# Kernel optimization log

Measured on AMD Instinct MI355X. Metric: run time of the kernel, lower is better.

The kernel has to match this reference:

```python
import jax, jax.numpy as jnp
import numpy as np
import math

B, S, H = 2, 2048, 4096
NH, HD = 32, 128            # num_heads, head_dim
Q_RANK, KV_RANK = 1536, 512 # low-rank dims
VD = 128                    # v_head_dim


def setup_inputs() -> dict:
    key = jax.random.key(0)
    ks = jax.random.split(key, 7)
    s = 0.02
    return {
        "hidden_states": jax.random.normal(ks[0], (B, S, H), dtype=jnp.float32),
        "w_qa":  jax.random.normal(ks[1], (H, Q_RANK), dtype=jnp.float32) * s,
        "w_qb":  jax.random.normal(ks[2], (Q_RANK, NH * HD), dtype=jnp.float32) * s,
        "w_kva": jax.random.normal(ks[3], (H, KV_RANK), dtype=jnp.float32) * s,
        "w_kb":  jax.random.normal(ks[4], (KV_RANK, NH * HD), dtype=jnp.float32) * s,
        "w_vb":  jax.random.normal(ks[5], (KV_RANK, NH * VD), dtype=jnp.float32) * s,
        "w_o":   jax.random.normal(ks[6], (NH * VD, H), dtype=jnp.float32) * s,
    }


def reference(hidden_states, w_qa, w_qb, w_kva, w_kb, w_vb, w_o):
    b, s, _ = hidden_states.shape
    # low-rank Q path
    q_c = hidden_states @ w_qa                       # [B,S,q_rank]
    q = (q_c @ w_qb).reshape(b, s, NH, HD)           # [B,S,NH,HD]
    # low-rank compressed KV (this is the cache tensor)
    compressed_kv = hidden_states @ w_kva            # [B,S,kv_rank]
    k = (compressed_kv @ w_kb).reshape(b, s, NH, HD)
    v = (compressed_kv @ w_vb).reshape(b, s, NH, VD)
    # causal SDPA, scale 1/sqrt(head_dim) (position_ids=None -> RoPE no-op)
    scale = 1.0 / math.sqrt(HD)
    scores = jnp.einsum('bqhd,bkhd->bhqk', q, k) * scale
    causal = jnp.tril(jnp.ones((s, s), dtype=bool))
    scores = jnp.where(causal, scores, jnp.finfo(scores.dtype).min)
    attn = jax.nn.softmax(scores, axis=-1)
    out = jnp.einsum('bhqk,bkhd->bqhd', attn, v).reshape(b, s, NH * VD)
    attn_output = out @ w_o                          # [B,S,H]
    return (attn_output, compressed_kv)
```

## Files before the change

### kernel.cpp

```cpp
#include <hip/hip_runtime.h>
#include <hip/hip_bf16.h>
#include <math.h>

#define BB 2
#define SS 2048
#define HH 4096
#define NHEADS 32
#define HDIM 128
#define VDIM 128
#define QRANK 1536
#define KVRANK 512
#define MROWS (BB * SS)

typedef unsigned short u16;
typedef unsigned int u32;
typedef short short8 __attribute__((ext_vector_type(8)));
typedef float floatx4 __attribute__((ext_vector_type(4)));

#if __has_builtin(__builtin_amdgcn_exp2f)
__device__ __forceinline__ float fast_exp2(float x) { return __builtin_amdgcn_exp2f(x); }
#else
__device__ __forceinline__ float fast_exp2(float x) { return exp2f(x); }
#endif

__device__ __forceinline__ u16 f2bf(float f) {
    u32 u = __float_as_uint(f);
    u += 0x7fffu + ((u >> 16) & 1u);
    return (u16)(u >> 16);
}

#define GLD16(gp, lp)                                                        \
    __builtin_amdgcn_global_load_lds(                                        \
        (const __attribute__((address_space(1))) void*)(gp),                 \
        (__attribute__((address_space(3))) void*)(lp), 16, 0, 0)

__global__ __launch_bounds__(256) void cvt_bf16(const float* __restrict__ in,
                                                u16* __restrict__ out, int n4) {
    int idx = blockIdx.x * 256 + threadIdx.x;
    int stride = gridDim.x * 256;
    for (int i = idx; i < n4; i += stride) {
        float4 f = ((const float4*)in)[i];
        u32 lo = (u32)f2bf(f.x) | ((u32)f2bf(f.y) << 16);
        u32 hi = (u32)f2bf(f.z) | ((u32)f2bf(f.w) << 16);
        ((uint2*)out)[i] = make_uint2(lo, hi);
    }
}

__global__ __launch_bounds__(256) void transpose_cvt(const float* __restrict__ in,
                                                     u16* __restrict__ out,
                                                     int R, int C) {
    __shared__ u16 T[64][65];
    const int c0 = blockIdx.x * 64, r0 = blockIdx.y * 64;
    const int tx = threadIdx.x & 63, ty = threadIdx.x >> 6;
#pragma unroll
    for (int p = 0; p < 16; ++p) {
        int rr = p * 4 + ty;
        T[rr][tx] = f2bf(in[(size_t)(r0 + rr) * C + c0 + tx]);
    }
    __syncthreads();
#pragma unroll
    for (int p = 0; p < 16; ++p) {
        int cc = p * 4 + ty;
        out[(size_t)(c0 + cc) * R + r0 + tx] = T[tx][cc];
    }
}

__global__ __launch_bounds__(256) void transpose_v(const u16* __restrict__ in, int ldin,
                                                   u16* __restrict__ out) {
    __shared__ u16 T[64][65];
    const int s0 = blockIdx.x * 64, d0 = blockIdx.y * 64;
    const int bh = blockIdx.z, b = bh >> 5, h = bh & 31;
    const int tx = threadIdx.x & 63, ty = threadIdx.x >> 6;
#pragma unroll
    for (int p = 0; p < 16; ++p) {
        int ss = p * 4 + ty;
        T[ss][tx] = in[(size_t)(b * SS + s0 + ss) * ldin + h * 128 + d0 + tx];
    }
    __syncthreads();
#pragma unroll
    for (int p = 0; p < 16; ++p) {
        int dd = p * 4 + ty;
        out[((size_t)bh * 128 + d0 + dd) * SS + s0 + tx] = T[tx][dd];
    }
}

template <int MODE>
__global__ __launch_bounds__(512) void gemm_bt(const u16* __restrict__ A, int lda,
                                               const u16* __restrict__ Bt, int ldb,
                                               float* __restrict__ Cf, int ldf,
                                               u16* __restrict__ Cb, int ldc,
                                               int M, int N, int K, int nsplit) {
    __shared__ __align__(16) u16 As[4][256 * 32];
    __shared__ __align__(16) u16 Bs[4][256 * 32];

    const int tid = threadIdx.x;
    const int bm0 = blockIdx.y * 256, bn0 = blockIdx.x * 256;
    const int w = tid >> 6, lane = tid & 63;
    const int lo = lane & 15, quad = lane >> 4;
    const int wm = (w >> 2) * 128, wn = (w & 3) * 64;

    floatx4 acc[8][4];
#pragma unroll
    for (int m = 0; m < 8; ++m)
#pragma unroll
        for (int n = 0; n < 4; ++n) acc[m][n] = (floatx4){0.f, 0.f, 0.f, 0.f};

    int row_[2], gco[2], ldso[2];
#pragma unroll
    for (int p = 0; p < 2; ++p) {
        int o = tid * 16 + p * 8192;
        row_[p] = o >> 6;
        int c = (o & 63) >> 4;
        gco[p] = ((c ^ ((row_[p] >> 1) & 3)) << 3);
        ldso[p] = o >> 1;
    }

    const u16* Ab = A + (size_t)bm0 * lda;
    const u16* Bb = Bt + (size_t)bn0 * ldb;
    const int NT = K >> 5;

    auto STAGE = [&](int t) {
        const int s = t & 3;
        const int k0 = t << 5;
#pragma unroll
        for (int p = 0; p < 2; ++p)
            GLD16(Ab + (size_t)row_[p] * lda + k0 + gco[p], &As[s][ldso[p]]);
#pragma unroll
        for (int p = 0; p < 2; ++p)
            GLD16(Bb + (size_t)row_[p] * ldb + k0 + gco[p], &Bs[s][ldso[p]]);
    };

    STAGE(0);
    if (NT > 1) STAGE(1);
    if (NT > 2) STAGE(2);

    for (int kt = 0; kt < NT; ++kt) {
        __builtin_amdgcn_s_barrier();
        if (kt + 3 < NT) STAGE(kt + 3);
        __builtin_amdgcn_sched_barrier(0);
        if (kt < NT - 3)       asm volatile("s_waitcnt vmcnt(12)" ::: "memory");
        else if (kt == NT - 3) asm volatile("s_waitcnt vmcnt(8)" ::: "memory");
        else if (kt == NT - 2) asm volatile("s_waitcnt vmcnt(4)" ::: "memory");
        else                   asm volatile("s_waitcnt vmcnt(0)" ::: "memory");
        __builtin_amdgcn_sched_barrier(0);
        __builtin_amdgcn_s_barrier();
        __builtin_amdgcn_sched_barrier(0);

        const int s = kt & 3;
        short8 af[8], bfr[4];
#pragma unroll
        for (int m = 0; m < 8; ++m) {
            const int r = wm + m * 16 + lo;
            af[m] = *(const short8*)&As[s][r * 32 + ((quad ^ ((r >> 1) & 3)) << 3)];
        }
#pragma unroll
        for (int n = 0; n < 4; ++n) {
            const int r = wn + n * 16 + lo;
            bfr[n] = *(const short8*)&Bs[s][r * 32 + ((quad ^ ((r >> 1) & 3)) << 3)];
        }
        __builtin_amdgcn_s_setprio(1);
#pragma unroll
        for (int m = 0; m < 8; ++m)
#pragma unroll
            for (int n = 0; n < 4; ++n)
                acc[m][n] = __builtin_amdgcn_mfma_f32_16x16x32_bf16(af[m], bfr[n], acc[m][n], 0, 0, 0);
        __builtin_amdgcn_s_setprio(0);
    }

#pragma unroll
    for (int m = 0; m < 8; ++m) {
#pragma unroll
        for (int n = 0; n < 4; ++n) {
            const int row = bm0 + wm + m * 16 + quad * 4;
            const int col = bn0 + wn + n * 16 + lo;
#pragma unroll
            for (int r = 0; r < 4; ++r) {
                float v = acc[m][n][r];
                if (MODE == 0) Cf[(size_t)(row + r) * ldf + col] = v;
                if (MODE == 1) Cb[(size_t)(row + r) * ldc + col] = f2bf(v);
                if (MODE == 3) {
                    Cb[(size_t)(row + r) * ldc + col] = f2bf(v);
                    if (col >= nsplit) Cf[(size_t)(row + r) * ldf + (col - nsplit)] = v;
                }
            }
        }
    }
}

__global__ __launch_bounds__(256) void mla_attn_mfma(const u16* __restrict__ qm,
                                                     const u16* __restrict__ km, int ldk,
                                                     const u16* __restrict__ vt,
                                                     u16* __restrict__ ao) {
    __shared__ __align__(16) u16 Ks[64 * 128];
    __shared__ __align__(16) u16 Vt[(128 + 16) * 64];
    __shared__ __align__(16) u16 Ps[128 * 68];

    const int qt = 15 - blockIdx.y;
    const int bh = blockIdx.x;
    const int b = bh >> 5, h = bh & 31;
    const int tid = threadIdx.x;
    const int w = tid >> 6, lane = tid & 63;
    const int lo = lane & 15, quad = lane >> 4;
    const int q0 = qt * 128;

    const float SCALE_L2E = 0.08838834764831845f * 1.4426950408889634f;

    {
        u32* p = (u32*)&Vt[128 * 64];
        for (int i = tid; i < 512; i += 256) p[i] = 0x3F803F80u;
    }

    const u16* kbase = km + (size_t)(b * SS) * ldk + h * 128;
    const u16* vtbase = vt + (size_t)bh * 128 * SS;
    const int nkt = 2 * qt + 2;

    int ol_[4], kgo[4], vgo[4];
#pragma unroll
    for (int p = 0; p < 4; ++p) {
        int o = tid * 16 + p * 4096;
        int key = o >> 8, ch = (o & 255) >> 4;
        kgo[p] = key * ldk + ((ch ^ (key & 15)) << 3);
        int d = o >> 7, ch2 = (o & 127) >> 4;
        vgo[p] = d * SS + ((ch2 ^ (d & 7)) << 3);
        ol_[p] = o >> 1;
    }

#pragma unroll
    for (int p = 0; p < 4; ++p) GLD16(kbase + kgo[p], &Ks[ol_[p]]);
#pragma unroll
    for (int p = 0; p < 4; ++p) GLD16(vtbase + vgo[p], &Vt[ol_[p]]);

    short8 qf[2][4];
#pragma unroll
    for (int mf = 0; mf < 2; ++mf) {
        const u16* qrow = qm + (size_t)(b * SS + q0 + w * 32 + mf * 16 + lo) * HH + h * 128;
#pragma unroll
        for (int ks = 0; ks < 4; ++ks) qf[mf][ks] = *(const short8*)(qrow + ks * 32 + quad * 8);
    }

    floatx4 oacc[2][8], olv[2];
#pragma unroll
    for (int mf = 0; mf < 2; ++mf) {
        olv[mf] = (floatx4){0.f, 0.f, 0.f, 0.f};
#pragma unroll
        for (int n = 0; n < 8; ++n) oacc[mf][n] = (floatx4){0.f, 0.f, 0.f, 0.f};
    }

    __syncthreads();

    for (int kt = 0; kt < nkt; ++kt) {
        const bool need_mask = (kt >= nkt - 2);
        const bool notlast = (kt + 1 < nkt);

#pragma unroll
        for (int mf = 0; mf < 2; ++mf) {
            floatx4 s[4];
#pragma unroll
            for (int nf = 0; nf < 4; ++nf) s[nf] = (floatx4){0.f, 0.f, 0.f, 0.f};
            __builtin_amdgcn_s_setprio(1);
#pragma unroll
            for (int nf = 0; nf < 4; ++nf)
#pragma unroll
                for (int ks = 0; ks < 4; ++ks) {
                    short8 kf = *(const short8*)&Ks[(nf * 16 + lo) * 128 + (((ks * 4 + quad) ^ lo) << 3)];
                    s[nf] = __builtin_amdgcn_mfma_f32_16x16x32_bf16(qf[mf][ks], kf, s[nf], 0, 0, 0);
                }
            __builtin_amdgcn_s_setprio(0);
#pragma unroll
            for (int nf = 0; nf < 4; ++nf)
#pragma unroll
                for (int r = 0; r < 4; ++r) {
                    float p = fast_exp2(s[nf][r] * SCALE_L2E);
                    if (need_mask) {
                        int kgi = kt * 64 + nf * 16 + lo;
                        int qg = q0 + w * 32 + mf * 16 + quad * 4 + r;
                        p = (kgi <= qg) ? p : 0.f;
                    }
                    Ps[(w * 32 + mf * 16 + quad * 4 + r) * 68 + nf * 16 + lo] = f2bf(p);
                }
        }

        __syncthreads();

        if (notlast) {
            const u16* kn = kbase + (size_t)(kt + 1) * 64 * ldk;
#pragma unroll
            for (int p = 0; p < 4; ++p) GLD16(kn + kgo[p], &Ks[ol_[p]]);
        }

#pragma unroll
        for (int mf = 0; mf < 2; ++mf) {
            short8 pa[2];
#pragma unroll
            for (int ks2 = 0; ks2 < 2; ++ks2)
                pa[ks2] = *(const short8*)&Ps[(w * 32 + mf * 16 + lo) * 68 + ks2 * 32 + quad * 8];
            __builtin_amdgcn_s_setprio(1);
#pragma unroll
            for (int n = 0; n < 8; ++n)
#pragma unroll
                for (int ks2 = 0; ks2 < 2; ++ks2) {
                    short8 vf = *(const short8*)&Vt[(n * 16 + lo) * 64 + (((ks2 * 4 + quad) ^ (lo & 7)) << 3)];
                    oacc[mf][n] = __builtin_amdgcn_mfma_f32_16x16x32_bf16(pa[ks2], vf, oacc[mf][n], 0, 0, 0);
                }
#pragma unroll
            for (int ks2 = 0; ks2 < 2; ++ks2) {
                short8 vf = *(const short8*)&Vt[(128 + lo) * 64 + (((ks2 * 4 + quad) ^ (lo & 7)) << 3)];
                olv[mf] = __builtin_amdgcn_mfma_f32_16x16x32_bf16(pa[ks2], vf, olv[mf], 0, 0, 0);
            }
            __builtin_amdgcn_s_setprio(0);
        }

        __syncthreads();

        if (notlast) {
            const u16* vn = vtbase + (size_t)(kt + 1) * 64;
#pragma unroll
            for (int p = 0; p < 4; ++p) GLD16(vn + vgo[p], &Vt[ol_[p]]);
        }
    }

#pragma unroll
    for (int mf = 0; mf < 2; ++mf) {
        u16* obase = ao + (size_t)(b * SS + q0 + w * 32 + mf * 16 + quad * 4) * HH + h * 128;
#pragma unroll
        for (int r = 0; r < 4; ++r) {
            float inv = 1.f / olv[mf][r];
#pragma unroll
            for (int n = 0; n < 8; ++n)
                obase[(size_t)r * HH + n * 16 + lo] = f2bf(oacc[mf][n][r] * inv);
        }
    }
}

extern "C" void kernel_launch(void* const* d_in, const int* in_sizes, int n_in,
                              void* d_out, int out_size, void* d_ws, size_t ws_size,
                              hipStream_t stream) {
    const float* hs    = (const float*)d_in[0];
    const float* w_qa  = (const float*)d_in[1];
    const float* w_qb  = (const float*)d_in[2];
    const float* w_kva = (const float*)d_in[3];
    const float* w_kb  = (const float*)d_in[4];
    const float* w_vb  = (const float*)d_in[5];
    const float* w_o   = (const float*)d_in[6];

    float* out   = (float*)d_out;
    float* ckv_f = out + (size_t)MROWS * HH;

    u16* ws = (u16*)d_ws;
    u16* hs_bf    = ws;
    u16* vt       = ws;
    u16* q_bf     = ws + 16777216ull;
    u16* kv_bf    = ws + 33554432ull;
    u16* ao_bf    = ws + 67108864ull;
    u16* wqa_kvaT = ws + 83886080ull;
    u16* w_qbT    = ws + 92274688ull;
    u16* wkv_bT   = ws + 98566144ull;
    u16* w_oT     = ws + 102760448ull;
    u16* qc_ckv   = ws + 119537664ull;

    dim3 blk(256);
    dim3 blkg(512);

    cvt_bf16<<<2048, blk, 0, stream>>>(hs, hs_bf, (MROWS * HH) / 4);
    transpose_cvt<<<dim3(QRANK / 64, HH / 64), blk, 0, stream>>>(w_qa, wqa_kvaT, HH, QRANK);
    transpose_cvt<<<dim3(KVRANK / 64, HH / 64), blk, 0, stream>>>(w_kva, wqa_kvaT + 1536ull * 4096, HH, KVRANK);
    transpose_cvt<<<dim3(HH / 64, QRANK / 64), blk, 0, stream>>>(w_qb, w_qbT, QRANK, HH);
    transpose_cvt<<<dim3(HH / 64, KVRANK / 64), blk, 0, stream>>>(w_kb, wkv_bT, KVRANK, HH);
    transpose_cvt<<<dim3(HH / 64, KVRANK / 64), blk, 0, stream>>>(w_vb, wkv_bT + 4096ull * 512, KVRANK, HH);
    transpose_cvt<<<dim3(HH / 64, HH / 64), blk, 0, stream>>>(w_o, w_oT, HH, HH);

    gemm_bt<3><<<dim3(2048 / 256, MROWS / 256), blkg, 0, stream>>>(
        hs_bf, HH, wqa_kvaT, HH, ckv_f, KVRANK, qc_ckv, 2048, MROWS, 2048, HH, QRANK);
    gemm_bt<1><<<dim3(HH / 256, MROWS / 256), blkg, 0, stream>>>(
        qc_ckv, 2048, w_qbT, QRANK, nullptr, 0, q_bf, HH, MROWS, HH, QRANK, 0);
    gemm_bt<1><<<dim3(8192 / 256, MROWS / 256), blkg, 0, stream>>>(
        qc_ckv + 1536, 2048, wkv_bT, KVRANK, nullptr, 0, kv_bf, 8192, MROWS, 8192, KVRANK, 0);
    transpose_v<<<dim3(SS / 64, VDIM / 64, BB * NHEADS), blk, 0, stream>>>(kv_bf + 4096, 8192, vt);
    mla_attn_mfma<<<dim3(BB * NHEADS, 16), blk, 0, stream>>>(q_bf, kv_bf, 8192, vt, ao_bf);
    gemm_bt<0><<<dim3(HH / 256, MROWS / 256), blkg, 0, stream>>>(
        ao_bf, HH, w_oT, HH, out, HH, nullptr, 0, MROWS, HH, HH, 0);
}
```

Measured before the change: 799.2 us.

## Restructure bf16 GEMM mainloop into 4-phase ping-pong with 64-wide K tiles

Measured after the change: 788.1 us. Within noise of the previous version (-1.4%).

```diff
diff --git a/kernel.cpp b/kernel.cpp
--- a/kernel.cpp
+++ b/kernel.cpp
@@ -84,19 +84,75 @@
     }
 }
 
+#define PHASE_BAR(NLIT)                                                          \
+    __builtin_amdgcn_sched_barrier(0);                                           \
+    asm volatile("s_waitcnt vmcnt(" NLIT ")\n\ts_barrier" ::: "memory");         \
+    __builtin_amdgcn_sched_barrier(0)
+
+#define MFMA_Q(AH, BH, AFR, BFR)                                                 \
+    __builtin_amdgcn_s_setprio(1);                                               \
+    _Pragma("unroll") for (int m_ = 0; m_ < 4; ++m_)                             \
+    _Pragma("unroll") for (int n_ = 0; n_ < 2; ++n_)                             \
+    _Pragma("unroll") for (int ks_ = 0; ks_ < 2; ++ks_)                          \
+        acc[m_ + (AH)*4][n_ + (BH)*2] = __builtin_amdgcn_mfma_f32_16x16x32_bf16( \
+            AFR[m_][ks_], BFR[n_][ks_], acc[m_ + (AH)*4][n_ + (BH)*2], 0, 0, 0); \
+    __builtin_amdgcn_s_setprio(0);                                               \
+    __builtin_amdgcn_sched_barrier(0)
+
+#define GTILE(T, WL)                                                              \
+    {                                                                             \
+        const int slot = (T) & 1;                                                 \
+        short8 a0[4][2], a1[4][2], b0[2][2], b1[2][2];                            \
+               \
+        _Pragma("unroll") for (int m_ = 0; m_ < 4; ++m_)                          \
+        _Pragma("unroll") for (int ks_ = 0; ks_ < 2; ++ks_)                       \
+            a0[m_][ks_] = *(const short8*)&As[slot][(wm + m_ * 16 + lo) * 64 +    \
+                                                    (((ks_ * 4 + quad) ^ lo7) << 3)]; \
+        _Pragma("unroll") for (int n_ = 0; n_ < 2; ++n_)                          \
+        _Pragma("unroll") for (int ks_ = 0; ks_ < 2; ++ks_)                       \
+            b0[n_][ks_] = *(const short8*)&Bs[slot][(wn + n_ * 16 + lo) * 64 +    \
+                                                    (((ks_ * 4 + quad) ^ lo7) << 3)]; \
+        if ((T) > 0 && (T) + 1 < NT) STAGE_A((T) + 1, 1);                         \
+        PHASE_BAR(WL);                                                            \
+        MFMA_Q(0, 0, a0, b0);                                                     \
+        asm volatile("s_waitcnt lgkmcnt(0)\n\ts_barrier" ::: "memory");           \
+        __builtin_amdgcn_sched_barrier(0);                                        \
+                       \
+        _Pragma("unroll") for (int n_ = 0; n_ < 2; ++n_)                          \
+        _Pragma("unroll") for (int ks_ = 0; ks_ < 2; ++ks_)                       \
+            b1[n_][ks_] = *(const short8*)&Bs[slot][(wn + 32 + n_ * 16 + lo) * 64 + \
+                                                    (((ks_ * 4 + quad) ^ lo7) << 3)]; \
+        if ((T) + 2 < NT) STAGE_A((T) + 2, 0);                                    \
+        PHASE_BAR(WL);                                                            \
+        MFMA_Q(0, 1, a0, b1);                                                     \
+                       \
+        _Pragma("unroll") for (int m_ = 0; m_ < 4; ++m_)                          \
+        _Pragma("unroll") for (int ks_ = 0; ks_ < 2; ++ks_)                       \
+            a1[m_][ks_] = *(const short8*)&As[slot][(wm + 64 + m_ * 16 + lo) * 64 + \
+                                                    (((ks_ * 4 + quad) ^ lo7) << 3)]; \
+        if ((T) + 2 < NT) STAGE_B((T) + 2, 0);                                    \
+        PHASE_BAR(WL);                                                            \
+        MFMA_Q(1, 0, a1, b0);                                                     \
+                                   \
+        if ((T) + 2 < NT) STAGE_B((T) + 2, 1);                                    \
+        PHASE_BAR(WL);                                                            \
+        MFMA_Q(1, 1, a1, b1);                                                     \
+    }
+
 template <int MODE>
 __global__ __launch_bounds__(512) void gemm_bt(const u16* __restrict__ A, int lda,
                                                const u16* __restrict__ Bt, int ldb,
                                                float* __restrict__ Cf, int ldf,
                                                u16* __restrict__ Cb, int ldc,
                                                int M, int N, int K, int nsplit) {
-    __shared__ __align__(16) u16 As[4][256 * 32];
-    __shared__ __align__(16) u16 Bs[4][256 * 32];
+    __shared__ __align__(16) u16 As[2][256 * 64];
+    __shared__ __align__(16) u16 Bs[2][256 * 64];
 
     const int tid = threadIdx.x;
     const int bm0 = blockIdx.y * 256, bn0 = blockIdx.x * 256;
     const int w = tid >> 6, lane = tid & 63;
     const int lo = lane & 15, quad = lane >> 4;
+    const int lo7 = lane & 7, l8 = lane >> 3;
     const int wm = (w >> 2) * 128, wn = (w & 3) * 64;
 
     floatx4 acc[8][4];
@@ -104,68 +160,50 @@
     for (int m = 0; m < 8; ++m)
 #pragma unroll
         for (int n = 0; n < 4; ++n) acc[m][n] = (floatx4){0.f, 0.f, 0.f, 0.f};
-
-    int row_[2], gco[2], ldso[2];
-#pragma unroll
-    for (int p = 0; p < 2; ++p) {
-        int o = tid * 16 + p * 8192;
-        row_[p] = o >> 6;
-        int c = (o & 63) >> 4;
-        gco[p] = ((c ^ ((row_[p] >> 1) & 3)) << 3);
-        ldso[p] = o >> 1;
-    }
 
     const u16* Ab = A + (size_t)bm0 * lda;
     const u16* Bb = Bt + (size_t)bn0 * ldb;
-    const int NT = K >> 5;
-
-    auto STAGE = [&](int t) {
-        const int s = t & 3;
-        const int k0 = t << 5;
+    const int NT = K >> 6;
+
+    const u16* aSrc[2][2]; const u16* bSrc[2][2];
+    int aDst[2][2], bDst[2][2];
+    const int csw = (lo7 ^ l8) << 3;
+#pragma unroll
+    for (int p = 0; p < 2; ++p) {
+        const int idx = w * 2 + p;
+#pragma unroll
+        for (int P = 0; P < 2; ++P) {
+            const int ra = (idx >> 3) * 128 + (idx & 7) * 8 + P * 64;
+            aSrc[P][p] = Ab + (size_t)(ra + l8) * lda + csw;
+            aDst[P][p] = ra * 64 + lane * 8;
+            const int rb = (idx >> 2) * 64 + (idx & 3) * 8 + P * 32;
+            bSrc[P][p] = Bb + (size_t)(rb + l8) * ldb + csw;
+            bDst[P][p] = rb * 64 + lane * 8;
+        }
+    }
+
+    auto STAGE_A = [&](int t, int P) {
+        const int s = t & 1;
 #pragma unroll
         for (int p = 0; p < 2; ++p)
-            GLD16(Ab + (size_t)row_[p] * lda + k0 + gco[p], &As[s][ldso[p]]);
+            GLD16(aSrc[P][p] + t * 64, &As[s][aDst[P][p]]);
+    };
+    auto STAGE_B = [&](int t, int P) {
+        const int s = t & 1;
 #pragma unroll
         for (int p = 0; p < 2; ++p)
-            GLD16(Bb + (size_t)row_[p] * ldb + k0 + gco[p], &Bs[s][ldso[p]]);
+            GLD16(bSrc[P][p] + t * 64, &Bs[s][bDst[P][p]]);
     };
 
-    STAGE(0);
-    if (NT > 1) STAGE(1);
-    if (NT > 2) STAGE(2);
-
-    for (int kt = 0; kt < NT; ++kt) {
-        __builtin_amdgcn_s_barrier();
-        if (kt + 3 < NT) STAGE(kt + 3);
-        __builtin_amdgcn_sched_barrier(0);
-        if (kt < NT - 3)       asm volatile("s_waitcnt vmcnt(12)" ::: "memory");
-        else if (kt == NT - 3) asm volatile("s_waitcnt vmcnt(8)" ::: "memory");
-        else if (kt == NT - 2) asm volatile("s_waitcnt vmcnt(4)" ::: "memory");
-        else                   asm volatile("s_waitcnt vmcnt(0)" ::: "memory");
-        __builtin_amdgcn_sched_barrier(0);
-        __builtin_amdgcn_s_barrier();
-        __builtin_amdgcn_sched_barrier(0);
-
-        const int s = kt & 3;
-        short8 af[8], bfr[4];
-#pragma unroll
-        for (int m = 0; m < 8; ++m) {
-            const int r = wm + m * 16 + lo;
-            af[m] = *(const short8*)&As[s][r * 32 + ((quad ^ ((r >> 1) & 3)) << 3)];
-        }
-#pragma unroll
-        for (int n = 0; n < 4; ++n) {
-            const int r = wn + n * 16 + lo;
-            bfr[n] = *(const short8*)&Bs[s][r * 32 + ((quad ^ ((r >> 1) & 3)) << 3)];
-        }
-        __builtin_amdgcn_s_setprio(1);
-#pragma unroll
-        for (int m = 0; m < 8; ++m)
-#pragma unroll
-            for (int n = 0; n < 4; ++n)
-                acc[m][n] = __builtin_amdgcn_mfma_f32_16x16x32_bf16(af[m], bfr[n], acc[m][n], 0, 0, 0);
-        __builtin_amdgcn_s_setprio(0);
-    }
+    STAGE_A(0, 0); STAGE_A(0, 1); STAGE_B(0, 0); STAGE_B(0, 1);
+    if (NT > 1) { STAGE_A(1, 0); STAGE_A(1, 1); STAGE_B(1, 0); STAGE_B(1, 1); }
+    asm volatile("s_waitcnt vmcnt(0)" ::: "memory");
+    __builtin_amdgcn_s_barrier();
+    __builtin_amdgcn_sched_barrier(0);
+
+    int t = 0;
+    for (; t + 2 < NT; ++t) GTILE(t, "10");
+    for (; t < NT; ++t) GTILE(t, "0");
 
 #pragma unroll
     for (int m = 0; m < 8; ++m) {
```

## Restructure GEMM mainloop into 8-phase ping-pong schedule with BK=64 tiles

Applied to the files above, without the earlier changes.

Result: faster. 693.4 us (-13.2%).

```diff
diff --git a/kernel.cpp b/kernel.cpp
--- a/kernel.cpp
+++ b/kernel.cpp
@@ -84,19 +84,33 @@
     }
 }
 
+#define BARRIER() asm volatile("s_barrier" ::: "memory")
+#define LGKM0()                                              \
+    asm volatile("s_waitcnt lgkmcnt(0)" ::: "memory");       \
+    __builtin_amdgcn_sched_barrier(0)
+#define MF16(MO, NO, AA, BB2)                                                     \
+    __builtin_amdgcn_s_setprio(1);                                                \
+    _Pragma("unroll") for (int m_ = 0; m_ < 4; ++m_)                              \
+    _Pragma("unroll") for (int n_ = 0; n_ < 2; ++n_)                              \
+    _Pragma("unroll") for (int k_ = 0; k_ < 2; ++k_)                              \
+        acc[m_ + (MO)][n_ + (NO)] = __builtin_amdgcn_mfma_f32_16x16x32_bf16(      \
+            AA[m_][k_], BB2[n_][k_], acc[m_ + (MO)][n_ + (NO)], 0, 0, 0);         \
+    __builtin_amdgcn_s_setprio(0)
+
 template <int MODE>
 __global__ __launch_bounds__(512) void gemm_bt(const u16* __restrict__ A, int lda,
                                                const u16* __restrict__ Bt, int ldb,
                                                float* __restrict__ Cf, int ldf,
                                                u16* __restrict__ Cb, int ldc,
                                                int M, int N, int K, int nsplit) {
-    __shared__ __align__(16) u16 As[4][256 * 32];
-    __shared__ __align__(16) u16 Bs[4][256 * 32];
+    __shared__ __align__(16) u16 As[2][256 * 64];
+    __shared__ __align__(16) u16 Bs[2][256 * 64];
 
     const int tid = threadIdx.x;
     const int bm0 = blockIdx.y * 256, bn0 = blockIdx.x * 256;
     const int w = tid >> 6, lane = tid & 63;
     const int lo = lane & 15, quad = lane >> 4;
+    const int lo7 = lane & 7, l8 = lane >> 3;
     const int wm = (w >> 2) * 128, wn = (w & 3) * 64;
 
     floatx4 acc[8][4];
@@ -104,67 +118,102 @@
     for (int m = 0; m < 8; ++m)
 #pragma unroll
         for (int n = 0; n < 4; ++n) acc[m][n] = (floatx4){0.f, 0.f, 0.f, 0.f};
-
-    int row_[2], gco[2], ldso[2];
-#pragma unroll
-    for (int p = 0; p < 2; ++p) {
-        int o = tid * 16 + p * 8192;
-        row_[p] = o >> 6;
-        int c = (o & 63) >> 4;
-        gco[p] = ((c ^ ((row_[p] >> 1) & 3)) << 3);
-        ldso[p] = o >> 1;
-    }
 
     const u16* Ab = A + (size_t)bm0 * lda;
     const u16* Bb = Bt + (size_t)bn0 * ldb;
-    const int NT = K >> 5;
-
-    auto STAGE = [&](int t) {
-        const int s = t & 3;
-        const int k0 = t << 5;
-#pragma unroll
-        for (int p = 0; p < 2; ++p)
-            GLD16(Ab + (size_t)row_[p] * lda + k0 + gco[p], &As[s][ldso[p]]);
-#pragma unroll
-        for (int p = 0; p < 2; ++p)
-            GLD16(Bb + (size_t)row_[p] * ldb + k0 + gco[p], &Bs[s][ldso[p]]);
+    const int NT = K >> 6;
+    const int csw = (lo7 ^ l8) << 3;
+
+    auto STAGE_A = [&](int s, int P, int tau) {
+#pragma unroll
+        for (int j = 0; j < 2; ++j) {
+            const int rb = P * 64 + j * 128 + w * 8;
+            GLD16(Ab + (size_t)(rb + l8) * lda + tau * 64 + csw, &As[s][rb * 64 + lane * 8]);
+        }
     };
-
-    STAGE(0);
-    if (NT > 1) STAGE(1);
-    if (NT > 2) STAGE(2);
-
-    for (int kt = 0; kt < NT; ++kt) {
-        __builtin_amdgcn_s_barrier();
-        if (kt + 3 < NT) STAGE(kt + 3);
-        __builtin_amdgcn_sched_barrier(0);
-        if (kt < NT - 3)       asm volatile("s_waitcnt vmcnt(12)" ::: "memory");
-        else if (kt == NT - 3) asm volatile("s_waitcnt vmcnt(8)" ::: "memory");
-        else if (kt == NT - 2) asm volatile("s_waitcnt vmcnt(4)" ::: "memory");
-        else                   asm volatile("s_waitcnt vmcnt(0)" ::: "memory");
-        __builtin_amdgcn_sched_barrier(0);
-        __builtin_amdgcn_s_barrier();
-        __builtin_amdgcn_sched_barrier(0);
-
-        const int s = kt & 3;
-        short8 af[8], bfr[4];
-#pragma unroll
-        for (int m = 0; m < 8; ++m) {
-            const int r = wm + m * 16 + lo;
-            af[m] = *(const short8*)&As[s][r * 32 + ((quad ^ ((r >> 1) & 3)) << 3)];
-        }
-#pragma unroll
-        for (int n = 0; n < 4; ++n) {
-            const int r = wn + n * 16 + lo;
-            bfr[n] = *(const short8*)&Bs[s][r * 32 + ((quad ^ ((r >> 1) & 3)) << 3)];
-        }
-        __builtin_amdgcn_s_setprio(1);
-#pragma unroll
-        for (int m = 0; m < 8; ++m)
-#pragma unroll
-            for (int n = 0; n < 4; ++n)
-                acc[m][n] = __builtin_amdgcn_mfma_f32_16x16x32_bf16(af[m], bfr[n], acc[m][n], 0, 0, 0);
-        __builtin_amdgcn_s_setprio(0);
+    auto STAGE_B = [&](int s, int P, int tau) {
+#pragma unroll
+        for (int j = 0; j < 2; ++j) {
+            const int rb = (w >> 2) * 64 + (w & 3) * 8 + P * 32 + j * 128;
+            GLD16(Bb + (size_t)(rb + l8) * ldb + tau * 64 + csw, &Bs[s][rb * 64 + lane * 8]);
+        }
+    };
+    auto RD_A = [&](short8 (&dst)[4][2], int s, int half) {
+#pragma unroll
+        for (int m = 0; m < 4; ++m)
+#pragma unroll
+            for (int ks = 0; ks < 2; ++ks) {
+                const int r = wm + half * 64 + m * 16 + lo;
+                dst[m][ks] = *(const short8*)&As[s][r * 64 + (((ks * 4 + quad) ^ lo7) << 3)];
+            }
+    };
+    auto RD_B = [&](short8 (&dst)[2][2], int s, int half) {
+#pragma unroll
+        for (int n = 0; n < 2; ++n)
+#pragma unroll
+            for (int ks = 0; ks < 2; ++ks) {
+                const int r = wn + half * 32 + n * 16 + lo;
+                dst[n][ks] = *(const short8*)&Bs[s][r * 64 + (((ks * 4 + quad) ^ lo7) << 3)];
+            }
+    };
+
+    STAGE_A(0, 0, 0); STAGE_A(0, 1, 0); STAGE_B(0, 0, 0); STAGE_B(0, 1, 0);
+    STAGE_A(1, 0, 1); STAGE_B(1, 0, 1); STAGE_B(1, 1, 1);
+    asm volatile("s_waitcnt vmcnt(6)" ::: "memory");
+    BARRIER();
+
+    for (int t = 0; t < NT; t += 2) {
+        const bool full = (t + 2 < NT);
+        short8 alo[4][2], ahi[4][2], blo[2][2], bhi[2][2];
+
+        RD_A(alo, 0, 0); RD_B(blo, 0, 0);
+        STAGE_A(1, 1, t + 1);
+        BARRIER(); LGKM0();
+        MF16(0, 0, alo, blo);
+        BARRIER();
+        RD_B(bhi, 0, 1);
+        if (full) STAGE_A(0, 0, t + 2);
+        BARRIER(); LGKM0();
+        MF16(0, 2, alo, bhi);
+        BARRIER();
+        RD_A(ahi, 0, 1);
+        if (full) STAGE_B(0, 0, t + 2);
+        BARRIER(); LGKM0();
+        MF16(4, 0, ahi, blo);
+        BARRIER();
+        if (full) {
+            STAGE_B(0, 1, t + 2);
+            asm volatile("s_waitcnt vmcnt(6)" ::: "memory");
+        } else {
+            asm volatile("s_waitcnt vmcnt(0)" ::: "memory");
+        }
+        BARRIER(); LGKM0();
+        MF16(4, 2, ahi, bhi);
+        BARRIER();
+        RD_A(alo, 1, 0); RD_B(blo, 1, 0);
+        if (full) STAGE_A(0, 1, t + 2);
+        BARRIER(); LGKM0();
+        MF16(0, 0, alo, blo);
+        BARRIER();
+        RD_B(bhi, 1, 1);
+        if (full) STAGE_A(1, 0, t + 3);
+        BARRIER(); LGKM0();
+        MF16(0, 2, alo, bhi);
+        BARRIER();
+        RD_A(ahi, 1, 1);
+        if (full) STAGE_B(1, 0, t + 3);
+        BARRIER(); LGKM0();
+        MF16(4, 0, ahi, blo);
+        BARRIER();
+        if (full) {
+            STAGE_B(1, 1, t + 3);
+            asm volatile("s_waitcnt vmcnt(6)" ::: "memory");
+        } else {
+            asm volatile("s_waitcnt vmcnt(0)" ::: "memory");
+        }
+        BARRIER(); LGKM0();
+        MF16(4, 2, ahi, bhi);
+        BARRIER();
     }
 
 #pragma unroll
```
